# Optimization experiments

Measured on AMD Instinct MI355X. Metric: run time of the kernel, lower is better.

## Reference

```python
import jax, jax.numpy as jnp
import numpy as np

B, L = 8, 2048
OBS, ACT = 64, 16
DM = 768          # d_model
DI = 2 * DM       # d_inner (expand=2)
N = 16            # d_state
R = 48            # dt_rank = ceil(d_model/16)
K = 4             # d_conv
NL = 2            # num_layers


def setup_inputs() -> dict:
    key = jax.random.key(0)
    ks = jax.random.split(key, 10)
    s = 0.02
    f32 = jnp.float32
    inp = {
        "obs": jax.random.normal(ks[0], (B, L, OBS), f32),
        "w_in": jax.random.normal(ks[1], (DM, OBS), f32) * s,
        "b_in": jnp.zeros((DM,), f32),
        "in_proj_w": jax.random.normal(ks[2], (NL, 2 * DI, DM), f32) * s,
        "conv_w": jax.random.normal(ks[3], (NL, DI, K), f32) * s,
        "conv_b": jnp.zeros((NL, DI), f32),
        "x_proj_w": jax.random.normal(ks[4], (NL, R + 2 * N, DI), f32) * s,
        "dt_proj_w": jax.random.normal(ks[5], (NL, DI, R), f32) * s,
        "dt_proj_b": jax.random.normal(ks[6], (NL, DI), f32) * s,
        "A_log": jnp.broadcast_to(jnp.log(jnp.arange(1, N + 1, dtype=f32)), (NL, DI, N)) + 0.0,
        "D_skip": jnp.ones((NL, DI), f32),
        "out_proj_w": jax.random.normal(ks[7], (NL, DM, DI), f32) * s,
        "w_out": jax.random.normal(ks[8], (ACT, DM), f32) * s,
        "b_out": jnp.zeros((ACT,), f32),
    }
    return inp


def selective_scan(x, dt, A, Bm, C, Dp):
    """x, dt: [B,L,DI]; A: [DI,N]; Bm, C: [B,L,N]; Dp: [DI]."""
    def step(h, inp):
        x_t, dt_t, B_t, C_t = inp  # [B,DI], [B,DI], [B,N], [B,N]
        dA = jnp.exp(dt_t[..., None] * A)                       # [B,DI,N]
        h = dA * h + (dt_t * x_t)[..., None] * B_t[:, None, :]  # [B,DI,N]
        y = jnp.einsum('bdn,bn->bd', h, C_t)
        return h, y

    h0 = jnp.zeros((x.shape[0], DI, N), x.dtype)
    xs = (jnp.swapaxes(x, 0, 1), jnp.swapaxes(dt, 0, 1),
          jnp.swapaxes(Bm, 0, 1), jnp.swapaxes(C, 0, 1))
    _, ys = jax.lax.scan(step, h0, xs)
    return jnp.swapaxes(ys, 0, 1) + x * Dp


def mamba_block(x, in_w, cw, cb, xp_w, dt_w, dt_b, A_log, Dp, out_w):
    xz = jnp.einsum('bld,ed->ble', x, in_w)   # [B,L,2*DI]
    xa, z = jnp.split(xz, 2, axis=-1)
    # causal depthwise conv, kernel K, left pad K-1
    xc = jax.lax.conv_general_dilated(
        jnp.swapaxes(xa, 1, 2), cw[:, None, :], (1,), [(K - 1, 0)],
        dimension_numbers=('NCH', 'OIH', 'NCH'), feature_group_count=DI)
    xa = jax.nn.silu(jnp.swapaxes(xc, 1, 2) + cb)
    x_dbl = jnp.einsum('bld,ed->ble', xa, xp_w)  # [B,L,R+2N]
    dt_r, Bm, C = jnp.split(x_dbl, [R, R + N], axis=-1)
    dt = jax.nn.softplus(jnp.einsum('blr,dr->bld', dt_r, dt_w) + dt_b)
    A = -jnp.exp(A_log)                          # [DI,N]
    y = selective_scan(xa, dt, A, Bm, C, Dp)
    y = y * jax.nn.silu(z)
    return jnp.einsum('bld,ed->ble', y, out_w)


def reference(obs, w_in, b_in, in_proj_w, conv_w, conv_b, x_proj_w,
              dt_proj_w, dt_proj_b, A_log, D_skip, out_proj_w, w_out, b_out):
    x = jnp.einsum('blo,do->bld', obs, w_in) + b_in
    for i in range(NL):
        x = mamba_block(x, in_proj_w[i], conv_w[i], conv_b[i], x_proj_w[i],
                        dt_proj_w[i], dt_proj_b[i], A_log[i], D_skip[i],
                        out_proj_w[i])
    return jnp.einsum('bld,ad->bla', x, w_out) + b_out
```

## Files before the change

### kernel.cpp

```cpp
#include <hip/hip_runtime.h>
#include <cstddef>

constexpr int Bb  = 8;
constexpr int Ll  = 2048;
constexpr int OBSn = 64;
constexpr int ACTn = 16;
constexpr int DMn = 768;
constexpr int DIn = 1536;
constexpr int Nn  = 16;
constexpr int Rn  = 48;
constexpr int Kc  = 4;
constexpr int NLn = 2;
constexpr int XD  = Rn + 2 * Nn;
constexpr int CH  = 64;
constexpr int NCH = Ll / CH;
constexpr int EOc = 2 * DIn;
constexpr float L2E = 1.4426950408889634f;

typedef __attribute__((ext_vector_type(8))) short short8v;
typedef __attribute__((ext_vector_type(4))) float f32x4;

__device__ inline ushort f2bf(float f) {
    uint u = __float_as_uint(f);
    return (ushort)((u + 0x7FFFu + ((u >> 16) & 1u)) >> 16);
}
__device__ inline float bf2f(ushort b) { return __uint_as_float(((uint)b) << 16); }
__device__ inline float exp2a(float x) {
    float r; asm("v_exp_f32 %0, %1" : "=v"(r) : "v"(x)); return r;
}

constexpr size_t WOFF_WIN = 0, WOFF_INP0 = 98304, WOFF_INP1 = 4816896,
                 WOFF_XP0 = 9535488, WOFF_XP1 = 9928704, WOFF_DT0 = 10321920,
                 WOFF_DT1 = 10518528, WOFF_OP0 = 10715136, WOFF_OP1 = 13074432,
                 WOFF_WOUT = 15433728, WTOT = 15630336;
constexpr size_t WQUADS = WTOT / 4;

__global__ __launch_bounds__(256)
void build_wsplit(const float* __restrict__ w_in, const float* __restrict__ inp,
                  const float* __restrict__ xp,  const float* __restrict__ dtp,
                  const float* __restrict__ op,  const float* __restrict__ wout,
                  ushort* __restrict__ WB)
{
    constexpr int NS = 10;
    constexpr int    sSel[NS] = {0,1,1,2,2,3,3,4,4,5};
    constexpr size_t sOff[NS] = {0, 0, 3072ull*768, 0, 80ull*1536, 0, 1536ull*48, 0, 768ull*1536, 0};
    constexpr int    sN[NS]   = {768,3072,3072,80,80,1536,1536,768,768,16};
    constexpr int    sK[NS]   = {64,768,768,1536,1536,48,48,1536,1536,768};
    constexpr int    sKp[NS]  = {64,768,768,1536,1536,64,64,1536,1536,768};
    constexpr size_t sD[NS]   = {WOFF_WIN,WOFF_INP0,WOFF_INP1,WOFF_XP0,WOFF_XP1,
                                 WOFF_DT0,WOFF_DT1,WOFF_OP0,WOFF_OP1,WOFF_WOUT};
    constexpr size_t sQ[NS+1] = {0,24576,1204224,2383872,2482176,2580480,
                                 2629632,2678784,3268608,3858432,3907584};

    size_t qid = (size_t)blockIdx.x * 256 + threadIdx.x;
    if (qid >= sQ[NS]) return;
    int s = 0;
#pragma unroll
    for (int i = 0; i < NS; ++i) if (qid >= sQ[i+1]) s = i + 1;

    size_t local = qid - sQ[s];
    const int Kp = sKp[s], K = sK[s], N = sN[s];
    const int ncol4 = (2 * Kp) >> 2;
    const int n  = (int)(local / ncol4);
    const int c4 = (int)(local % ncol4) * 4;
    const bool lo = (c4 >= Kp);
    const int sc = lo ? c4 - Kp : c4;
    ushort4 o; o.x = o.y = o.z = o.w = 0;
    if (n < N && sc < K) {
        const float* src;
        switch (sSel[s]) { case 0: src = w_in; break; case 1: src = inp; break;
                           case 2: src = xp;   break; case 3: src = dtp; break;
                           case 4: src = op;   break; default: src = wout; }
        float4 v = *reinterpret_cast<const float4*>(src + sOff[s] + (size_t)n * K + sc);
        ushort h0 = f2bf(v.x), h1 = f2bf(v.y), h2 = f2bf(v.z), h3 = f2bf(v.w);
        if (lo) {
            h0 = f2bf(v.x - bf2f(h0)); h1 = f2bf(v.y - bf2f(h1));
            h2 = f2bf(v.z - bf2f(h2)); h3 = f2bf(v.w - bf2f(h3));
        }
        o.x = h0; o.y = h1; o.z = h2; o.w = h3;
    }
    *reinterpret_cast<ushort4*>(WB + sD[s] + (size_t)n * (2 * Kp) + c4) = o;
}

__global__ __launch_bounds__(256)
void build_bf(const float* __restrict__ src, ushort* __restrict__ dst, int n4)
{
    int i = blockIdx.x * 256 + threadIdx.x;
    if (i >= n4) return;
    float4 v = *reinterpret_cast<const float4*>(src + (size_t)i * 4);
    ushort4 o; o.x = f2bf(v.x); o.y = f2bf(v.y); o.z = f2bf(v.z); o.w = f2bf(v.w);
    *reinterpret_cast<ushort4*>(dst + (size_t)i * 4) = o;
}

template<int BM, int OUT, int SPLITK, bool WLO = true>
__global__ __launch_bounds__(256)
void gemm_ws(const ushort* __restrict__ Ap, int lda,
             const ushort* __restrict__ Wp,
             const float* __restrict__ bias,
             float* __restrict__ Cf, ushort* __restrict__ Cb, int ldc,
             int M, int N, int Kp, int ktLen)
{
    constexpr int MI = BM / 32;
    __shared__ ushort As[BM * 32];
    __shared__ ushort Ws2[WLO ? 8192 : 4096];

    const int nwgx = gridDim.x;
    const int nwg  = nwgx * gridDim.y;
    int bid = blockIdx.y * nwgx + blockIdx.x;
    {
        int q = nwg >> 3, r = nwg & 7;
        int x = bid & 7, lc = bid >> 3;
        bid = (x < r ? x * (q + 1) : r * (q + 1) + (x - r) * q) + lc;
    }
    const int col0 = (bid % nwgx) * 128;
    const int row0 = (bid / nwgx) * BM;

    const int tid = threadIdx.x, w = tid >> 6, lane = tid & 63;
    const int wr = w >> 1, wc = w & 1, half = lane >> 4, lid = lane & 15;

    f32x4 acc[MI][4];
#pragma unroll
    for (int i = 0; i < MI; ++i)
#pragma unroll
        for (int j = 0; j < 4; ++j) acc[i][j] = (f32x4){0.f, 0.f, 0.f, 0.f};

    const int gr = lane >> 2, gc8 = (lane & 3) * 8;
    const int ldw = 2 * Kp;
    const int kt0 = SPLITK ? blockIdx.z * ktLen : 0;

    for (int kt = kt0; kt < kt0 + ktLen; kt += 32) {
        if constexpr (BM == 128) {
#pragma unroll
            for (int j = 0; j < 2; ++j) {
                int g = w * 2 + j;
                __builtin_amdgcn_global_load_lds(
                    (const __attribute__((address_space(1))) uint*)(Ap + (size_t)(row0 + g*16 + gr) * lda + kt + gc8),
                    (__attribute__((address_space(3))) uint*)(&As[g * 512]), 16, 0, 0);
            }
        } else {
            int g = w;
            __builtin_amdgcn_global_load_lds(
                (const __attribute__((address_space(1))) uint*)(Ap + (size_t)(row0 + g*16 + gr) * lda + kt + gc8),
                (__attribute__((address_space(3))) uint*)(&As[g * 512]), 16, 0, 0);
        }
#pragma unroll
        for (int j = 0; j < 2; ++j) {
            int g = w * 2 + j;
            const ushort* wsrc = Wp + (size_t)(col0 + g*16 + gr) * ldw + kt + gc8;
            __builtin_amdgcn_global_load_lds(
                (const __attribute__((address_space(1))) uint*)wsrc,
                (__attribute__((address_space(3))) uint*)(&Ws2[g * 512]), 16, 0, 0);
            if constexpr (WLO)
                __builtin_amdgcn_global_load_lds(
                    (const __attribute__((address_space(1))) uint*)(wsrc + Kp),
                    (__attribute__((address_space(3))) uint*)(&Ws2[4096 + g * 512]), 16, 0, 0);
        }
        __syncthreads();

        short8v a[MI], bh[4];
#pragma unroll
        for (int mi = 0; mi < MI; ++mi)
            a[mi] = *reinterpret_cast<const short8v*>(&As[(wr*(BM/2) + mi*16 + lid) * 32 + half * 8]);
#pragma unroll
        for (int ni = 0; ni < 4; ++ni)
            bh[ni] = *reinterpret_cast<const short8v*>(&Ws2[(wc*64 + ni*16 + lid) * 32 + half * 8]);
#pragma unroll
        for (int mi = 0; mi < MI; ++mi)
#pragma unroll
            for (int ni = 0; ni < 4; ++ni)
                acc[mi][ni] = __builtin_amdgcn_mfma_f32_16x16x32_bf16(a[mi], bh[ni], acc[mi][ni], 0, 0, 0);
        if constexpr (WLO) {
            short8v bl[4];
#pragma unroll
            for (int ni = 0; ni < 4; ++ni)
                bl[ni] = *reinterpret_cast<const short8v*>(&Ws2[4096 + (wc*64 + ni*16 + lid) * 32 + half * 8]);
#pragma unroll
            for (int mi = 0; mi < MI; ++mi)
#pragma unroll
                for (int ni = 0; ni < 4; ++ni)
                    acc[mi][ni] = __builtin_amdgcn_mfma_f32_16x16x32_bf16(a[mi], bl[ni], acc[mi][ni], 0, 0, 0);
        }
        __syncthreads();
    }

    if constexpr (SPLITK) {
        float* P = Cf + (size_t)blockIdx.z * M * 128;
#pragma unroll
        for (int mi = 0; mi < MI; ++mi) {
            int r = row0 + wr*(BM/2) + mi*16 + half*4;
#pragma unroll
            for (int ni = 0; ni < 4; ++ni) {
                int c = col0 + wc*64 + ni*16 + lid;
#pragma unroll
                for (int q = 0; q < 4; ++q)
                    P[(size_t)(r + q) * 128 + c] = acc[mi][ni][q];
            }
        }
    } else {
#pragma unroll
        for (int mi = 0; mi < MI; ++mi) {
            int r = row0 + wr*(BM/2) + mi*16 + half*4;
#pragma unroll
            for (int ni = 0; ni < 4; ++ni) {
                int c = col0 + wc*64 + ni*16 + lid;
                if (c >= N) continue;
                float bv = bias ? bias[c] : 0.f;
#pragma unroll
                for (int q = 0; q < 4; ++q) {
                    float v = acc[mi][ni][q] + bv;
                    if constexpr (OUT == 2 || OUT == 4) v = (v > 20.f) ? v : log1pf(__expf(v));
                    if constexpr (OUT == 1 || OUT == 4) Cb[(size_t)(r + q) * ldc + c] = f2bf(v);
                    else                                Cf[(size_t)(r + q) * ldc + c] = v;
                }
            }
        }
    }
}

__global__ __launch_bounds__(256)
void reduce_sk(const float* __restrict__ P, int S, int M,
               const float* __restrict__ bias,
               float* __restrict__ Cf, int ldc, int N,
               ushort* __restrict__ Cb, int nbf, int nbfPad,
               float* __restrict__ Bcp)
{
    int idx = blockIdx.x * 256 + threadIdx.x;
    if (idx >= M * 128) return;
    int c = idx & 127, r = idx >> 7;
    float v = 0.f;
    for (int s = 0; s < S; ++s) v += P[(size_t)s * M * 128 + idx];
    if (bias) v += bias[c];
    if (Cf && c < N) Cf[(size_t)r * ldc + c] = v;
    if (Cb && c < nbfPad) Cb[(size_t)r * nbfPad + c] = (c < nbf) ? f2bf(v) : (ushort)0;
    if (Bcp && c >= Rn && c < Rn + 2 * Nn) Bcp[(size_t)r * 32 + (c - Rn)] = v;
}

__global__ __launch_bounds__(256)
void conv_silu(const ushort* __restrict__ xz, const float* __restrict__ cw,
               const float* __restrict__ cb, ushort* __restrict__ xo, int rowsTotal)
{
    constexpr int ND4 = DIn / 4;
    int idx = blockIdx.x * 256 + threadIdx.x;
    if (idx >= rowsTotal * ND4) return;
    int d4 = (idx % ND4) * 4, row = idx / ND4, l = row % Ll;
    float4 cbv = *reinterpret_cast<const float4*>(cb + d4);
    float acc[4] = {cbv.x, cbv.y, cbv.z, cbv.w};
    float4 w0 = *reinterpret_cast<const float4*>(cw + (d4 + 0) * 4);
    float4 w1 = *reinterpret_cast<const float4*>(cw + (d4 + 1) * 4);
    float4 w2 = *reinterpret_cast<const float4*>(cw + (d4 + 2) * 4);
    float4 w3 = *reinterpret_cast<const float4*>(cw + (d4 + 3) * 4);
    const float* wv[4] = {(const float*)&w0, (const float*)&w1,
                          (const float*)&w2, (const float*)&w3};
#pragma unroll
    for (int j = 0; j < Kc; ++j) {
        int lo = l - 3 + j;
        if (lo >= 0) {
            ushort4 xv = *reinterpret_cast<const ushort4*>(xz + (size_t)(row - 3 + j) * EOc + d4);
            acc[0] = fmaf(wv[0][j], bf2f(xv.x), acc[0]);
            acc[1] = fmaf(wv[1][j], bf2f(xv.y), acc[1]);
            acc[2] = fmaf(wv[2][j], bf2f(xv.z), acc[2]);
            acc[3] = fmaf(wv[3][j], bf2f(xv.w), acc[3]);
        }
    }
    ushort4 o;
    o.x = f2bf(acc[0] * __builtin_amdgcn_rcpf(1.f + exp2a(-acc[0] * L2E)));
    o.y = f2bf(acc[1] * __builtin_amdgcn_rcpf(1.f + exp2a(-acc[1] * L2E)));
    o.z = f2bf(acc[2] * __builtin_amdgcn_rcpf(1.f + exp2a(-acc[2] * L2E)));
    o.w = f2bf(acc[3] * __builtin_amdgcn_rcpf(1.f + exp2a(-acc[3] * L2E)));
    *reinterpret_cast<ushort4*>(xo + (size_t)row * DIn + d4) = o;
}

__global__ __launch_bounds__(256)
void scan_pass1(const ushort* __restrict__ dtb, const ushort* __restrict__ xab,
                const float* __restrict__ bcp, const float* __restrict__ A_log,
                float* __restrict__ hend, float* __restrict__ Pbuf, int BC)
{
    int idx = blockIdx.x * 256 + threadIdx.x;
    if (idx >= BC * DIn * NCH * 2) return;
    int ng = idx & 1;
    int rest = idx >> 1;
    int d = rest % DIn;
    int t = rest / DIn;
    int c = t % NCH, b = t / NCH;

    float A2[8];
    {
        float4 a0 = *reinterpret_cast<const float4*>(A_log + d * Nn + ng * 8);
        float4 a1 = *reinterpret_cast<const float4*>(A_log + d * Nn + ng * 8 + 4);
        A2[0] = -__expf(a0.x) * L2E; A2[1] = -__expf(a0.y) * L2E;
        A2[2] = -__expf(a0.z) * L2E; A2[3] = -__expf(a0.w) * L2E;
        A2[4] = -__expf(a1.x) * L2E; A2[5] = -__expf(a1.y) * L2E;
        A2[6] = -__expf(a1.z) * L2E; A2[7] = -__expf(a1.w) * L2E;
    }
    float h[8] = {0.f,0.f,0.f,0.f,0.f,0.f,0.f,0.f};
    float S = 0.f;

    const size_t row0 = (size_t)b * Ll + c * CH;
    const ushort* pdt = dtb + row0 * DIn + d;
    const ushort* px  = xab + row0 * DIn + d;
    const float*  pb  = bcp + row0 * 32 + ng * 8;

    float dtv = bf2f(*pdt);
    float xv  = bf2f(*px);
    float4 b0 = *reinterpret_cast<const float4*>(pb);
    float4 b1 = *reinterpret_cast<const float4*>(pb + 4);

    for (int l = 0; l < CH; ++l) {
        pdt += DIn; px += DIn; pb += 32;
        float dtn = bf2f(*pdt);
        float xn  = bf2f(*px);
        float4 bn0 = *reinterpret_cast<const float4*>(pb);
        float4 bn1 = *reinterpret_cast<const float4*>(pb + 4);
        float cx = dtv * xv;
        S += dtv;
        float bb[8] = {b0.x,b0.y,b0.z,b0.w,b1.x,b1.y,b1.z,b1.w};
#pragma unroll
        for (int k = 0; k < 8; ++k) {
            float dA = exp2a(dtv * A2[k]);
            h[k] = fmaf(dA, h[k], cx * bb[k]);
        }
        dtv = dtn; xv = xn; b0 = bn0; b1 = bn1;
    }
    size_t o = (size_t)rest * Nn + ng * 8;
    *reinterpret_cast<float4*>(hend + o)     = (float4){h[0],h[1],h[2],h[3]};
    *reinterpret_cast<float4*>(hend + o + 4) = (float4){h[4],h[5],h[6],h[7]};
    *reinterpret_cast<float4*>(Pbuf + o) =
        (float4){exp2a(A2[0]*S), exp2a(A2[1]*S), exp2a(A2[2]*S), exp2a(A2[3]*S)};
    *reinterpret_cast<float4*>(Pbuf + o + 4) =
        (float4){exp2a(A2[4]*S), exp2a(A2[5]*S), exp2a(A2[6]*S), exp2a(A2[7]*S)};
}

__global__ __launch_bounds__(256)
void scan_pass2(const float* __restrict__ hend, const float* __restrict__ Pbuf,
                float* __restrict__ hstart, int BC)
{
    int idx = blockIdx.x * 256 + threadIdx.x;
    if (idx >= BC * DIn * Nn) return;
    int n = idx % Nn;
    int d = (idx / Nn) % DIn;
    int b = idx / (Nn * DIn);
    float hs = 0.f;
    for (int c = 0; c < NCH; ++c) {
        size_t o = (((size_t)b * NCH + c) * DIn + d) * Nn + n;
        hstart[o] = hs;
        hs = fmaf(Pbuf[o], hs, hend[o]);
    }
}

__global__ __launch_bounds__(256)
void scan_pass3(const ushort* __restrict__ dtb, ushort* __restrict__ xab,
                const float* __restrict__ bcp, const float* __restrict__ A_log,
                const float* __restrict__ Dp, const ushort* __restrict__ xzb,
                const float* __restrict__ hstart, int BC)
{
    int idx = blockIdx.x * 256 + threadIdx.x;
    if (idx >= BC * DIn * NCH * 2) return;
    int ng = idx & 1;
    int rest = idx >> 1;
    int d = rest % DIn;
    int t = rest / DIn;
    int c = t % NCH, b = t / NCH;

    float A2[8];
    {
        float4 a0 = *reinterpret_cast<const float4*>(A_log + d * Nn + ng * 8);
        float4 a1 = *reinterpret_cast<const float4*>(A_log + d * Nn + ng * 8 + 4);
        A2[0] = -__expf(a0.x) * L2E; A2[1] = -__expf(a0.y) * L2E;
        A2[2] = -__expf(a0.z) * L2E; A2[3] = -__expf(a0.w) * L2E;
        A2[4] = -__expf(a1.x) * L2E; A2[5] = -__expf(a1.y) * L2E;
        A2[6] = -__expf(a1.z) * L2E; A2[7] = -__expf(a1.w) * L2E;
    }
    float h[8];
    {
        float4 h0 = *reinterpret_cast<const float4*>(hstart + (size_t)rest * Nn + ng * 8);
        float4 h1 = *reinterpret_cast<const float4*>(hstart + (size_t)rest * Nn + ng * 8 + 4);
        h[0]=h0.x; h[1]=h0.y; h[2]=h0.z; h[3]=h0.w;
        h[4]=h1.x; h[5]=h1.y; h[6]=h1.z; h[7]=h1.w;
    }
    const float Dd = Dp[d];

    const size_t row0 = (size_t)b * Ll + c * CH;
    const ushort* pdt = dtb + row0 * DIn + d;
    ushort*       px  = xab + row0 * DIn + d;
    const ushort* pz  = xzb + row0 * EOc + DIn + d;
    const float*  pb  = bcp + row0 * 32 + ng * 8;
    const float*  pc  = bcp + row0 * 32 + 16 + ng * 8;

    float dtv = bf2f(*pdt);
    float xv  = bf2f(*px);
    float zv  = bf2f(*pz);
    float4 b0 = *reinterpret_cast<const float4*>(pb);
    float4 b1 = *reinterpret_cast<const float4*>(pb + 4);
    float4 c0 = *reinterpret_cast<const float4*>(pc);
    float4 c1 = *reinterpret_cast<const float4*>(pc + 4);

    for (int l = 0; l < CH; ++l) {
        float dtn = bf2f(pdt[DIn]);
        float xn  = bf2f(px[DIn]);
        float zn  = bf2f(pz[EOc]);
        float4 bn0 = *reinterpret_cast<const float4*>(pb + 32);
        float4 bn1 = *reinterpret_cast<const float4*>(pb + 36);
        float4 cn0 = *reinterpret_cast<const float4*>(pc + 32);
        float4 cn1 = *reinterpret_cast<const float4*>(pc + 36);
        float cx = dtv * xv;
        float bb[8] = {b0.x,b0.y,b0.z,b0.w,b1.x,b1.y,b1.z,b1.w};
        float cc[8] = {c0.x,c0.y,c0.z,c0.w,c1.x,c1.y,c1.z,c1.w};
        float y = 0.f;
#pragma unroll
        for (int k = 0; k < 8; ++k) {
            float dA = exp2a(dtv * A2[k]);
            h[k] = fmaf(dA, h[k], cx * bb[k]);
            y = fmaf(h[k], cc[k], y);
        }
        y += __shfl_xor(y, 1);
        y = fmaf(xv, Dd, y);
        float sz = zv * __builtin_amdgcn_rcpf(1.f + exp2a(-zv * L2E));
        if (ng == 0) *px = f2bf(y * sz);
        dtv = dtn; xv = xn; zv = zn; b0 = bn0; b1 = bn1; c0 = cn0; c1 = cn1;
        pdt += DIn; px += DIn; pz += EOc; pb += 32; pc += 32;
    }
}

extern "C" void kernel_launch(void* const* d_in, const int* in_sizes, int n_in,
                              void* d_out, int out_size, void* d_ws, size_t ws_size,
                              hipStream_t stream)
{
    const float* obs        = (const float*)d_in[0];
    const float* w_in       = (const float*)d_in[1];
    const float* b_in       = (const float*)d_in[2];
    const float* in_proj_w  = (const float*)d_in[3];
    const float* conv_w     = (const float*)d_in[4];
    const float* conv_b     = (const float*)d_in[5];
    const float* x_proj_w   = (const float*)d_in[6];
    const float* dt_proj_w  = (const float*)d_in[7];
    const float* dt_proj_b  = (const float*)d_in[8];
    const float* A_log      = (const float*)d_in[9];
    const float* D_skip     = (const float*)d_in[10];
    const float* out_proj_w = (const float*)d_in[11];
    const float* w_out      = (const float*)d_in[12];
    const float* b_out      = (const float*)d_in[13];
    float* out = (float*)d_out;

    auto aux_bc   = []() -> size_t { return 3ull * DIn * NCH * Nn * 4; };
    auto parts_bc = []() -> size_t { return 4ull * Ll * 128 * 4; };
    auto per_bc = [&]() -> size_t {
        size_t r = Ll;
        size_t bts = r*EOc*2
                   + r*DIn*2
                   + r*DIn*2
                   + r*32*4
                   + r*64*2
                   + r*DMn*2
                   + r*OBSn*2;
        size_t shared = aux_bc() > parts_bc() ? aux_bc() : parts_bc();
        return bts + shared + 8192;
    };
    const size_t wbytes = WTOT * 2 + 1024;
    int BC = 8;
    while (BC > 1 && wbytes + per_bc() * BC > ws_size) BC >>= 1;

    ushort* WB = (ushort*)d_ws;
    build_wsplit<<<(int)((WQUADS + 255) / 256), 256, 0, stream>>>(
        w_in, in_proj_w, x_proj_w, dt_proj_w, out_proj_w, w_out, WB);

    const size_t WLAY_INP[2] = {WOFF_INP0, WOFF_INP1};
    const size_t WLAY_XP[2]  = {WOFF_XP0,  WOFF_XP1};
    const size_t WLAY_DT[2]  = {WOFF_DT0,  WOFF_DT1};
    const size_t WLAY_OP[2]  = {WOFF_OP0,  WOFF_OP1};

    for (int b0 = 0; b0 < Bb; b0 += BC) {
        const int M = BC * Ll;
        char* base = (char*)d_ws + ((wbytes + 255) & ~(size_t)255);
        auto alloc = [&](size_t bytes) -> char* {
            char* r = base; base += (bytes + 255) & ~(size_t)255; return r;
        };
        ushort* xzb   = (ushort*)alloc((size_t)M * EOc * 2);
        ushort* xab   = (ushort*)alloc((size_t)M * DIn * 2);
        ushort* dtbb  = (ushort*)alloc((size_t)M * DIn * 2);
        float*  bcp   = (float*) alloc((size_t)M * 32 * 4);
        ushort* dtr   = (ushort*)alloc((size_t)M * 64 * 2);
        ushort* xbuf  = (ushort*)alloc((size_t)M * DMn * 2);
        ushort* obsb  = (ushort*)alloc((size_t)M * OBSn * 2);
        const size_t sseg = (size_t)BC * DIn * NCH * Nn;
        size_t shared_bytes = 3 * sseg * 4;
        if ((size_t)BC * parts_bc() > shared_bytes) shared_bytes = (size_t)BC * parts_bc();
        char* shared = alloc(shared_bytes);
        float* parts = (float*)shared;
        float* hend  = (float*)shared;
        float* Pb    = (float*)(shared + sseg * 4);
        float* hst   = (float*)(shared + 2 * sseg * 4);

        build_bf<<<(M * OBSn / 4 + 255) / 256, 256, 0, stream>>>(
            obs + (size_t)b0 * Ll * OBSn, obsb, M * OBSn / 4);
        gemm_ws<64, 1, 0><<<dim3(6, M / 64), 256, 0, stream>>>(
            obsb, OBSn, WB + WOFF_WIN, b_in, nullptr, xbuf, DMn, M, DMn, 64, 64);

        for (int layer = 0; layer < NLn; ++layer) {
            const float* cw     = conv_w    + (size_t)layer * DIn * Kc;
            const float* cb     = conv_b    + (size_t)layer * DIn;
            const float* dtbias = dt_proj_b + (size_t)layer * DIn;
            const float* Al     = A_log     + (size_t)layer * DIn * Nn;
            const float* Dpp    = D_skip    + (size_t)layer * DIn;

            gemm_ws<128, 1, 0, false><<<dim3(24, M / 128), 256, 0, stream>>>(
                xbuf, DMn, WB + WLAY_INP[layer], nullptr, nullptr, xzb, EOc, M, EOc, DMn, DMn);
            conv_silu<<<(M * (DIn / 4) + 255) / 256, 256, 0, stream>>>(xzb, cw, cb, xab, M);
            gemm_ws<64, 0, 1><<<dim3(1, M / 64, 4), 256, 0, stream>>>(
                xab, DIn, WB + WLAY_XP[layer], nullptr, parts, nullptr, 128, M, 128, DIn, DIn / 4);
            reduce_sk<<<(M * 128 + 255) / 256, 256, 0, stream>>>(
                parts, 4, M, nullptr, nullptr, 0, 0, dtr, Rn, 64, bcp);
            gemm_ws<64, 4, 0><<<dim3(12, M / 64), 256, 0, stream>>>(
                dtr, 64, WB + WLAY_DT[layer], dtbias, nullptr, dtbb, DIn, M, DIn, 64, 64);
            {
                int tot1 = BC * DIn * NCH * 2;
                scan_pass1<<<(tot1 + 255) / 256, 256, 0, stream>>>(dtbb, xab, bcp, Al, hend, Pb, BC);
                int tot2 = BC * DIn * Nn;
                scan_pass2<<<(tot2 + 255) / 256, 256, 0, stream>>>(hend, Pb, hst, BC);
                scan_pass3<<<(tot1 + 255) / 256, 256, 0, stream>>>(dtbb, xab, bcp, Al, Dpp, xzb, hst, BC);
            }
            gemm_ws<64, 1, 0, false><<<dim3(6, M / 64), 256, 0, stream>>>(
                xab, DIn, WB + WLAY_OP[layer], nullptr, nullptr, xbuf, DMn, M, DMn, DIn, DIn);
        }
        gemm_ws<64, 0, 1><<<dim3(1, M / 64, 4), 256, 0, stream>>>(
            xbuf, DMn, WB + WOFF_WOUT, nullptr, parts, nullptr, 128, M, 128, DMn, DMn / 4);
        reduce_sk<<<(M * 128 + 255) / 256, 256, 0, stream>>>(
            parts, 4, M, b_out, out + (size_t)b0 * Ll * ACTn, ACTn, ACTn, nullptr, 0, 0, nullptr);
    }
}
```

Measured before the change: 1.331 ms.

## Split in_proj output into separate xa/z buffers and restructure chunked scan

The in_proj GEMM now writes the xa and z halves into separate contiguous DIn-wide buffers, reusing the dt buffer as a temporary for xa, so conv and scan read dense rows instead of striding across the 2*DI layout. The scan kernels switch from two threads per channel (8 states each, with a shuffle reduction) to one thread per channel holding all 16 states. The chunk length is halved to restore parallelism, and pass2 writes the chunk start states in place over the decay buffer, dropping one scratch array. The trade-off is more register pressure per scan thread and more chunks for pass2 to walk sequentially.

```diff
diff --git a/kernel.cpp b/kernel.cpp
--- a/kernel.cpp
+++ b/kernel.cpp
@@ -12,7 +12,7 @@
 constexpr int Kc  = 4;
 constexpr int NLn = 2;
 constexpr int XD  = Rn + 2 * Nn;
-constexpr int CH  = 64;
+constexpr int CH  = 32;
 constexpr int NCH = Ll / CH;
 constexpr int EOc = 2 * DIn;
 constexpr float L2E = 1.4426950408889634f;
@@ -97,7 +97,8 @@
 void gemm_ws(const ushort* __restrict__ Ap, int lda,
              const ushort* __restrict__ Wp,
              const float* __restrict__ bias,
-             float* __restrict__ Cf, ushort* __restrict__ Cb, int ldc,
+             float* __restrict__ Cf, ushort* __restrict__ Cb,
+             ushort* __restrict__ Cb2, int ldc,
              int M, int N, int Kp, int ktLen)
 {
     constexpr int MI = BM / 32;
@@ -196,6 +197,22 @@
                     P[(size_t)(r + q) * 128 + c] = acc[mi][ni][q];
             }
         }
+    } else if constexpr (OUT == 3) {
+#pragma unroll
+        for (int mi = 0; mi < MI; ++mi) {
+            int r = row0 + wr*(BM/2) + mi*16 + half*4;
+#pragma unroll
+            for (int ni = 0; ni < 4; ++ni) {
+                int c = col0 + wc*64 + ni*16 + lid;
+                if (c < DIn) {
+#pragma unroll
+                    for (int q = 0; q < 4; ++q) Cb[(size_t)(r + q) * ldc + c] = f2bf(acc[mi][ni][q]);
+                } else {
+#pragma unroll
+                    for (int q = 0; q < 4; ++q) Cb2[(size_t)(r + q) * ldc + (c - DIn)] = f2bf(acc[mi][ni][q]);
+                }
+            }
+        }
     } else {
 #pragma unroll
         for (int mi = 0; mi < MI; ++mi) {
@@ -236,7 +253,7 @@
 }
 
 __global__ __launch_bounds__(256)
-void conv_silu(const ushort* __restrict__ xz, const float* __restrict__ cw,
+void conv_silu(const ushort* __restrict__ xi, const float* __restrict__ cw,
                const float* __restrict__ cb, ushort* __restrict__ xo, int rowsTotal)
 {
     constexpr int ND4 = DIn / 4;
@@ -255,7 +272,7 @@
     for (int j = 0; j < Kc; ++j) {
         int lo = l - 3 + j;
         if (lo >= 0) {
-            ushort4 xv = *reinterpret_cast<const ushort4*>(xz + (size_t)(row - 3 + j) * EOc + d4);
+            ushort4 xv = *reinterpret_cast<const ushort4*>(xi + (size_t)(row - 3 + j) * DIn + d4);
             acc[0] = fmaf(wv[0][j], bf2f(xv.x), acc[0]);
             acc[1] = fmaf(wv[1][j], bf2f(xv.y), acc[1]);
             acc[2] = fmaf(wv[2][j], bf2f(xv.z), acc[2]);
@@ -276,63 +293,65 @@
                 float* __restrict__ hend, float* __restrict__ Pbuf, int BC)
 {
     int idx = blockIdx.x * 256 + threadIdx.x;
-    if (idx >= BC * DIn * NCH * 2) return;
-    int ng = idx & 1;
-    int rest = idx >> 1;
-    int d = rest % DIn;
-    int t = rest / DIn;
+    if (idx >= BC * DIn * NCH) return;
+    int d = idx % DIn;
+    int t = idx / DIn;
     int c = t % NCH, b = t / NCH;
 
-    float A2[8];
-    {
-        float4 a0 = *reinterpret_cast<const float4*>(A_log + d * Nn + ng * 8);
-        float4 a1 = *reinterpret_cast<const float4*>(A_log + d * Nn + ng * 8 + 4);
-        A2[0] = -__expf(a0.x) * L2E; A2[1] = -__expf(a0.y) * L2E;
-        A2[2] = -__expf(a0.z) * L2E; A2[3] = -__expf(a0.w) * L2E;
-        A2[4] = -__expf(a1.x) * L2E; A2[5] = -__expf(a1.y) * L2E;
-        A2[6] = -__expf(a1.z) * L2E; A2[7] = -__expf(a1.w) * L2E;
-    }
-    float h[8] = {0.f,0.f,0.f,0.f,0.f,0.f,0.f,0.f};
+    float A2[16];
+#pragma unroll
+    for (int q = 0; q < 4; ++q) {
+        float4 a = *reinterpret_cast<const float4*>(A_log + d * Nn + q * 4);
+        A2[q*4+0] = -__expf(a.x) * L2E; A2[q*4+1] = -__expf(a.y) * L2E;
+        A2[q*4+2] = -__expf(a.z) * L2E; A2[q*4+3] = -__expf(a.w) * L2E;
+    }
+    float h[16];
+#pragma unroll
+    for (int k = 0; k < 16; ++k) h[k] = 0.f;
     float S = 0.f;
 
     const size_t row0 = (size_t)b * Ll + c * CH;
     const ushort* pdt = dtb + row0 * DIn + d;
     const ushort* px  = xab + row0 * DIn + d;
-    const float*  pb  = bcp + row0 * 32 + ng * 8;
+    const float*  pb  = bcp + row0 * 32;
 
     float dtv = bf2f(*pdt);
     float xv  = bf2f(*px);
-    float4 b0 = *reinterpret_cast<const float4*>(pb);
-    float4 b1 = *reinterpret_cast<const float4*>(pb + 4);
 
     for (int l = 0; l < CH; ++l) {
-        pdt += DIn; px += DIn; pb += 32;
+        pdt += DIn; px += DIn;
         float dtn = bf2f(*pdt);
         float xn  = bf2f(*px);
-        float4 bn0 = *reinterpret_cast<const float4*>(pb);
-        float4 bn1 = *reinterpret_cast<const float4*>(pb + 4);
+        float4 b0 = *reinterpret_cast<const float4*>(pb);
+        float4 b1 = *reinterpret_cast<const float4*>(pb + 4);
+        float4 b2 = *reinterpret_cast<const float4*>(pb + 8);
+        float4 b3 = *reinterpret_cast<const float4*>(pb + 12);
+        pb += 32;
         float cx = dtv * xv;
         S += dtv;
-        float bb[8] = {b0.x,b0.y,b0.z,b0.w,b1.x,b1.y,b1.z,b1.w};
-#pragma unroll
-        for (int k = 0; k < 8; ++k) {
+        float bb[16] = {b0.x,b0.y,b0.z,b0.w, b1.x,b1.y,b1.z,b1.w,
+                        b2.x,b2.y,b2.z,b2.w, b3.x,b3.y,b3.z,b3.w};
+#pragma unroll
+        for (int k = 0; k < 16; ++k) {
             float dA = exp2a(dtv * A2[k]);
             h[k] = fmaf(dA, h[k], cx * bb[k]);
         }
-        dtv = dtn; xv = xn; b0 = bn0; b1 = bn1;
-    }
-    size_t o = (size_t)rest * Nn + ng * 8;
-    *reinterpret_cast<float4*>(hend + o)     = (float4){h[0],h[1],h[2],h[3]};
-    *reinterpret_cast<float4*>(hend + o + 4) = (float4){h[4],h[5],h[6],h[7]};
-    *reinterpret_cast<float4*>(Pbuf + o) =
-        (float4){exp2a(A2[0]*S), exp2a(A2[1]*S), exp2a(A2[2]*S), exp2a(A2[3]*S)};
-    *reinterpret_cast<float4*>(Pbuf + o + 4) =
-        (float4){exp2a(A2[4]*S), exp2a(A2[5]*S), exp2a(A2[6]*S), exp2a(A2[7]*S)};
-}
-
-__global__ __launch_bounds__(256)
-void scan_pass2(const float* __restrict__ hend, const float* __restrict__ Pbuf,
-                float* __restrict__ hstart, int BC)
+        dtv = dtn; xv = xn;
+    }
+    size_t o = (size_t)idx * Nn;
+#pragma unroll
+    for (int q = 0; q < 4; ++q)
+        *reinterpret_cast<float4*>(hend + o + q * 4) =
+            (float4){h[q*4], h[q*4+1], h[q*4+2], h[q*4+3]};
+#pragma unroll
+    for (int q = 0; q < 4; ++q)
+        *reinterpret_cast<float4*>(Pbuf + o + q * 4) =
+            (float4){exp2a(A2[q*4]*S), exp2a(A2[q*4+1]*S),
+                     exp2a(A2[q*4+2]*S), exp2a(A2[q*4+3]*S)};
+}
+
+__global__ __launch_bounds__(256)
+void scan_pass2(const float* __restrict__ hend, float* __restrict__ Pbuf, int BC)
 {
     int idx = blockIdx.x * 256 + threadIdx.x;
     if (idx >= BC * DIn * Nn) return;
@@ -340,84 +359,82 @@
     int d = (idx / Nn) % DIn;
     int b = idx / (Nn * DIn);
     float hs = 0.f;
+#pragma unroll 4
     for (int c = 0; c < NCH; ++c) {
         size_t o = (((size_t)b * NCH + c) * DIn + d) * Nn + n;
-        hstart[o] = hs;
-        hs = fmaf(Pbuf[o], hs, hend[o]);
+        float P  = Pbuf[o];
+        float he = hend[o];
+        Pbuf[o] = hs;
+        hs = fmaf(P, hs, he);
     }
 }
 
 __global__ __launch_bounds__(256)
 void scan_pass3(const ushort* __restrict__ dtb, ushort* __restrict__ xab,
                 const float* __restrict__ bcp, const float* __restrict__ A_log,
-                const float* __restrict__ Dp, const ushort* __restrict__ xzb,
+                const float* __restrict__ Dp, const ushort* __restrict__ zb,
                 const float* __restrict__ hstart, int BC)
 {
     int idx = blockIdx.x * 256 + threadIdx.x;
-    if (idx >= BC * DIn * NCH * 2) return;
-    int ng = idx & 1;
-    int rest = idx >> 1;
-    int d = rest % DIn;
-    int t = rest / DIn;
+    if (idx >= BC * DIn * NCH) return;
+    int d = idx % DIn;
+    int t = idx / DIn;
     int c = t % NCH, b = t / NCH;
 
-    float A2[8];
-    {
-        float4 a0 = *reinterpret_cast<const float4*>(A_log + d * Nn + ng * 8);
-        float4 a1 = *reinterpret_cast<const float4*>(A_log + d * Nn + ng * 8 + 4);
-        A2[0] = -__expf(a0.x) * L2E; A2[1] = -__expf(a0.y) * L2E;
-        A2[2] = -__expf(a0.z) * L2E; A2[3] = -__expf(a0.w) * L2E;
-        A2[4] = -__expf(a1.x) * L2E; A2[5] = -__expf(a1.y) * L2E;
-        A2[6] = -__expf(a1.z) * L2E; A2[7] = -__expf(a1.w) * L2E;
-    }
-    float h[8];
-    {
-        float4 h0 = *reinterpret_cast<const float4*>(hstart + (size_t)rest * Nn + ng * 8);
-        float4 h1 = *reinterpret_cast<const float4*>(hstart + (size_t)rest * Nn + ng * 8 + 4);
-        h[0]=h0.x; h[1]=h0.y; h[2]=h0.z; h[3]=h0.w;
-        h[4]=h1.x; h[5]=h1.y; h[6]=h1.z; h[7]=h1.w;
+    float A2[16];
+#pragma unroll
+    for (int q = 0; q < 4; ++q) {
+        float4 a = *reinterpret_cast<const float4*>(A_log + d * Nn + q * 4);
+        A2[q*4+0] = -__expf(a.x) * L2E; A2[q*4+1] = -__expf(a.y) * L2E;
+        A2[q*4+2] = -__expf(a.z) * L2E; A2[q*4+3] = -__expf(a.w) * L2E;
+    }
+    float h[16];
+#pragma unroll
+    for (int q = 0; q < 4; ++q) {
+        float4 hv = *reinterpret_cast<const float4*>(hstart + (size_t)idx * Nn + q * 4);
+        h[q*4] = hv.x; h[q*4+1] = hv.y; h[q*4+2] = hv.z; h[q*4+3] = hv.w;
     }
     const float Dd = Dp[d];
 
     const size_t row0 = (size_t)b * Ll + c * CH;
     const ushort* pdt = dtb + row0 * DIn + d;
     ushort*       px  = xab + row0 * DIn + d;
-    const ushort* pz  = xzb + row0 * EOc + DIn + d;
-    const float*  pb  = bcp + row0 * 32 + ng * 8;
-    const float*  pc  = bcp + row0 * 32 + 16 + ng * 8;
+    const ushort* pz  = zb  + row0 * DIn + d;
 
     float dtv = bf2f(*pdt);
     float xv  = bf2f(*px);
     float zv  = bf2f(*pz);
-    float4 b0 = *reinterpret_cast<const float4*>(pb);
-    float4 b1 = *reinterpret_cast<const float4*>(pb + 4);
-    float4 c0 = *reinterpret_cast<const float4*>(pc);
-    float4 c1 = *reinterpret_cast<const float4*>(pc + 4);
+    const float* pb = bcp + row0 * 32;
 
     for (int l = 0; l < CH; ++l) {
         float dtn = bf2f(pdt[DIn]);
         float xn  = bf2f(px[DIn]);
-        float zn  = bf2f(pz[EOc]);
-        float4 bn0 = *reinterpret_cast<const float4*>(pb + 32);
-        float4 bn1 = *reinterpret_cast<const float4*>(pb + 36);
-        float4 cn0 = *reinterpret_cast<const float4*>(pc + 32);
-        float4 cn1 = *reinterpret_cast<const float4*>(pc + 36);
+        float zn  = bf2f(pz[DIn]);
+        float4 b0 = *reinterpret_cast<const float4*>(pb);
+        float4 b1 = *reinterpret_cast<const float4*>(pb + 4);
+        float4 b2 = *reinterpret_cast<const float4*>(pb + 8);
+        float4 b3 = *reinterpret_cast<const float4*>(pb + 12);
+        float4 c0 = *reinterpret_cast<const float4*>(pb + 16);
+        float4 c1 = *reinterpret_cast<const float4*>(pb + 20);
+        float4 c2 = *reinterpret_cast<const float4*>(pb + 24);
+        float4 c3 = *reinterpret_cast<const float4*>(pb + 28);
         float cx = dtv * xv;
-        float bb[8] = {b0.x,b0.y,b0.z,b0.w,b1.x,b1.y,b1.z,b1.w};
-        float cc[8] = {c0.x,c0.y,c0.z,c0.w,c1.x,c1.y,c1.z,c1.w};
+        float bb[16] = {b0.x,b0.y,b0.z,b0.w, b1.x,b1.y,b1.z,b1.w,
+                        b2.x,b2.y,b2.z,b2.w, b3.x,b3.y,b3.z,b3.w};
+        float cc[16] = {c0.x,c0.y,c0.z,c0.w, c1.x,c1.y,c1.z,c1.w,
+                        c2.x,c2.y,c2.z,c2.w, c3.x,c3.y,c3.z,c3.w};
         float y = 0.f;
 #pragma unroll
-        for (int k = 0; k < 8; ++k) {
+        for (int k = 0; k < 16; ++k) {
             float dA = exp2a(dtv * A2[k]);
             h[k] = fmaf(dA, h[k], cx * bb[k]);
             y = fmaf(h[k], cc[k], y);
         }
-        y += __shfl_xor(y, 1);
         y = fmaf(xv, Dd, y);
         float sz = zv * __builtin_amdgcn_rcpf(1.f + exp2a(-zv * L2E));
-        if (ng == 0) *px = f2bf(y * sz);
-        dtv = dtn; xv = xn; zv = zn; b0 = bn0; b1 = bn1; c0 = cn0; c1 = cn1;
-        pdt += DIn; px += DIn; pz += EOc; pb += 32; pc += 32;
+        *px = f2bf(y * sz);
+        dtv = dtn; xv = xn; zv = zn;
+        pdt += DIn; px += DIn; pz += DIn; pb += 32;
     }
 }
 
@@ -441,11 +458,11 @@
     const float* b_out      = (const float*)d_in[13];
     float* out = (float*)d_out;
 
-    auto aux_bc   = []() -> size_t { return 3ull * DIn * NCH * Nn * 4; };
+    auto aux_bc   = []() -> size_t { return 2ull * DIn * NCH * Nn * 4; };
     auto parts_bc = []() -> size_t { return 4ull * Ll * 128 * 4; };
     auto per_bc = [&]() -> size_t {
         size_t r = Ll;
-        size_t bts = r*EOc*2
+        size_t bts = r*DIn*2
                    + r*DIn*2
                    + r*DIn*2
                    + r*32*4
@@ -474,7 +491,7 @@
         auto alloc = [&](size_t bytes) -> char* {
             char* r = base; base += (bytes + 255) & ~(size_t)255; return r;
         };
-        ushort* xzb   = (ushort*)alloc((size_t)M * EOc * 2);
+        ushort* zb    = (ushort*)alloc((size_t)M * DIn * 2);
         ushort* xab   = (ushort*)alloc((size_t)M * DIn * 2);
         ushort* dtbb  = (ushort*)alloc((size_t)M * DIn * 2);
         float*  bcp   = (float*) alloc((size_t)M * 32 * 4);
@@ -482,18 +499,17 @@
         ushort* xbuf  = (ushort*)alloc((size_t)M * DMn * 2);
         ushort* obsb  = (ushort*)alloc((size_t)M * OBSn * 2);
         const size_t sseg = (size_t)BC * DIn * NCH * Nn;
-        size_t shared_bytes = 3 * sseg * 4;
+        size_t shared_bytes = 2 * sseg * 4;
         if ((size_t)BC * parts_bc() > shared_bytes) shared_bytes = (size_t)BC * parts_bc();
         char* shared = alloc(shared_bytes);
         float* parts = (float*)shared;
         float* hend  = (float*)shared;
         float* Pb    = (float*)(shared + sseg * 4);
-        float* hst   = (float*)(shared + 2 * sseg * 4);
 
         build_bf<<<(M * OBSn / 4 + 255) / 256, 256, 0, stream>>>(
             obs + (size_t)b0 * Ll * OBSn, obsb, M * OBSn / 4);
         gemm_ws<64, 1, 0><<<dim3(6, M / 64), 256, 0, stream>>>(
-            obsb, OBSn, WB + WOFF_WIN, b_in, nullptr, xbuf, DMn, M, DMn, 64, 64);
+            obsb, OBSn, WB + WOFF_WIN, b_in, nullptr, xbuf, nullptr, DMn, M, DMn, 64, 64);
 
         for (int layer = 0; layer < NLn; ++layer) {
             const float* cw     = conv_w    + (size_t)layer * DIn * Kc;
@@ -501,28 +517,29 @@
             const float* dtbias = dt_proj_b + (size_t)layer * DIn;
             const float* Al     = A_log     + (size_t)layer * DIn * Nn;
             const float* Dpp    = D_skip    + (size_t)layer * DIn;
-
-            gemm_ws<128, 1, 0, false><<<dim3(24, M / 128), 256, 0, stream>>>(
-                xbuf, DMn, WB + WLAY_INP[layer], nullptr, nullptr, xzb, EOc, M, EOc, DMn, DMn);
-            conv_silu<<<(M * (DIn / 4) + 255) / 256, 256, 0, stream>>>(xzb, cw, cb, xab, M);
+            ushort* xa_tmp = dtbb;
+
+            gemm_ws<128, 3, 0, false><<<dim3(24, M / 128), 256, 0, stream>>>(
+                xbuf, DMn, WB + WLAY_INP[layer], nullptr, nullptr, xa_tmp, zb, DIn, M, EOc, DMn, DMn);
+            conv_silu<<<(M * (DIn / 4) + 255) / 256, 256, 0, stream>>>(xa_tmp, cw, cb, xab, M);
             gemm_ws<64, 0, 1><<<dim3(1, M / 64, 4), 256, 0, stream>>>(
-                xab, DIn, WB + WLAY_XP[layer], nullptr, parts, nullptr, 128, M, 128, DIn, DIn / 4);
+                xab, DIn, WB + WLAY_XP[layer], nullptr, parts, nullptr, nullptr, 128, M, 128, DIn, DIn / 4);
             reduce_sk<<<(M * 128 + 255) / 256, 256, 0, stream>>>(
                 parts, 4, M, nullptr, nullptr, 0, 0, dtr, Rn, 64, bcp);
             gemm_ws<64, 4, 0><<<dim3(12, M / 64), 256, 0, stream>>>(
-                dtr, 64, WB + WLAY_DT[layer], dtbias, nullptr, dtbb, DIn, M, DIn, 64, 64);
+                dtr, 64, WB + WLAY_DT[layer], dtbias, nullptr, dtbb, nullptr, DIn, M, DIn, 64, 64);
             {
-                int tot1 = BC * DIn * NCH * 2;
+                int tot1 = BC * DIn * NCH;
                 scan_pass1<<<(tot1 + 255) / 256, 256, 0, stream>>>(dtbb, xab, bcp, Al, hend, Pb, BC);
                 int tot2 = BC * DIn * Nn;
-                scan_pass2<<<(tot2 + 255) / 256, 256, 0, stream>>>(hend, Pb, hst, BC);
-                scan_pass3<<<(tot1 + 255) / 256, 256, 0, stream>>>(dtbb, xab, bcp, Al, Dpp, xzb, hst, BC);
+                scan_pass2<<<(tot2 + 255) / 256, 256, 0, stream>>>(hend, Pb, BC);
+                scan_pass3<<<(tot1 + 255) / 256, 256, 0, stream>>>(dtbb, xab, bcp, Al, Dpp, zb, Pb, BC);
             }
             gemm_ws<64, 1, 0, false><<<dim3(6, M / 64), 256, 0, stream>>>(
-                xab, DIn, WB + WLAY_OP[layer], nullptr, nullptr, xbuf, DMn, M, DMn, DIn, DIn);
+                xab, DIn, WB + WLAY_OP[layer], nullptr, nullptr, xbuf, nullptr, DMn, M, DMn, DIn, DIn);
         }
         gemm_ws<64, 0, 1><<<dim3(1, M / 64, 4), 256, 0, stream>>>(
-            xbuf, DMn, WB + WOFF_WOUT, nullptr, parts, nullptr, 128, M, 128, DMn, DMn / 4);
+            xbuf, DMn, WB + WOFF_WOUT, nullptr, parts, nullptr, nullptr, 128, M, 128, DMn, DMn / 4);
         reduce_sk<<<(M * 128 + 255) / 256, 256, 0, stream>>>(
             parts, 4, M, b_out, out + (size_t)b0 * Ll * ACTn, ACTn, ACTn, nullptr, 0, 0, nullptr);
     }
```

After: 1.332 ms. Within noise of the previous version (+0.0%).
